# Optimization experiments

Measured on AMD Instinct MI355X. Metric: run time of the kernel, lower is better.

Reference implementation:

```python
import jax, jax.numpy as jnp
import numpy as np

V, D, H, NL, C, CD, B, L = 50257, 512, 8, 4, 10, 64, 16, 512
DH = D // H
EPS = 1e-5


def layer_norm(x, g, b):
    m = jnp.mean(x, axis=-1, keepdims=True)
    v = jnp.var(x, axis=-1, keepdims=True)
    return (x - m) * jax.lax.rsqrt(v + EPS) * g + b


def setup_inputs() -> dict:
    key = jax.random.key(0)
    ks = jax.random.split(key, 16)
    s = lambda k, shape: (jax.random.normal(k, shape, jnp.float32) * 0.02)
    x = jax.random.randint(ks[0], (B, L), 0, V, dtype=jnp.int32)
    return {
        "x": x,
        "embed": s(ks[1], (V, D)),
        "pos": jax.random.normal(ks[2], (1, L, D), jnp.float32),  # nn.Parameter randn
        "Wqkv": s(ks[3], (NL, 3 * D, D)), "bqkv": jnp.zeros((NL, 3 * D)),
        "Wo": s(ks[4], (NL, D, D)), "bo": jnp.zeros((NL, D)),
        "ln1_g": jnp.ones((NL, D)), "ln1_b": jnp.zeros((NL, D)),
        "W1": s(ks[5], (NL, 4 * D, D)), "b1": jnp.zeros((NL, 4 * D)),
        "W2": s(ks[6], (NL, D, 4 * D)), "b2": jnp.zeros((NL, D)),
        "ln2_g": jnp.ones((NL, D)), "ln2_b": jnp.zeros((NL, D)),
        "cnt_ln_g": jnp.ones((V,)), "cnt_ln_b": jnp.zeros((V,)),
        "Wc": s(ks[7], (CD, V)), "bc": jnp.zeros((CD,)),
        "Wh": s(ks[8], (C, D + CD)), "bh": jnp.zeros((C,)),
    }


def _encoder(x, embed, pos, Wqkv, bqkv, Wo, bo, ln1_g, ln1_b, W1, b1, W2, b2, ln2_g, ln2_b):
    h = embed[x] + pos[:, : x.shape[1]]  # (B,L,D)
    scale = 1.0 / jnp.sqrt(jnp.float32(DH))
    for i in range(NL):
        # post-LN TransformerEncoderLayer, gelu (exact), dropout=0 (eval)
        qkv = h @ Wqkv[i].T + bqkv[i]
        q, k, v = jnp.split(qkv, 3, axis=-1)
        q = q.reshape(B, L, H, DH)
        k = k.reshape(B, L, H, DH)
        v = v.reshape(B, L, H, DH)
        att = jax.nn.softmax(jnp.einsum("bqhd,bkhd->bhqk", q, k) * scale, axis=-1)
        o = jnp.einsum("bhqk,bkhd->bqhd", att, v).reshape(B, L, D)
        h = layer_norm(h + o @ Wo[i].T + bo[i], ln1_g[i], ln1_b[i])
        ff = jax.nn.gelu(h @ W1[i].T + b1[i], approximate=False) @ W2[i].T + b2[i]
        h = layer_norm(h + ff, ln2_g[i], ln2_b[i])
    return h


def reference(x, embed, pos, Wqkv, bqkv, Wo, bo, ln1_g, ln1_b, W1, b1, W2, b2,
              ln2_g, ln2_b, cnt_ln_g, cnt_ln_b, Wc, bc, Wh, bh):
    enc = _encoder(x, embed, pos, Wqkv, bqkv, Wo, bo, ln1_g, ln1_b, W1, b1, W2, b2, ln2_g, ln2_b)
    ctx_vec = enc.mean(axis=1)  # (B,D)
    # histogram of tokens per sequence, pad (id 0) excluded: same math as
    # one_hot(x).masked_fill(x==pad).sum(1) but O(B*L) scatter-add.
    mask = (x != 0).astype(jnp.float32)
    counts = jnp.zeros((B, V), jnp.float32).at[jnp.arange(B)[:, None], x].add(mask)
    cf = jax.nn.relu(layer_norm(counts, cnt_ln_g, cnt_ln_b) @ Wc.T + bc)  # (B,CD)
    feat = jnp.concatenate([ctx_vec, cf], axis=-1)
    return feat @ Wh.T + bh  # (B,C)
```

## Files before the change

kernel.cpp:

```cpp
#include <hip/hip_runtime.h>
#include <hip/hip_bf16.h>
#include <math.h>

#define V_  50257
#define D_  512
#define H_  8
#define NL_ 4
#define C_  10
#define CD_ 64
#define B_  16
#define L_  512
#define DH_ 64

typedef __attribute__((ext_vector_type(8))) short bf16x8;
typedef __attribute__((ext_vector_type(4))) float f32x4;

__device__ inline float bf2f(unsigned short u) {
    union { unsigned int i; float f; } c; c.i = ((unsigned int)u) << 16; return c.f;
}
__device__ inline unsigned short f2bf(float f) {
    unsigned int x = __float_as_uint(f);
    unsigned int r = (x + 0x7fffu + ((x >> 16) & 1u)) >> 16;
    return (unsigned short)r;
}
__device__ inline unsigned long long pack4(float a, float b, float c, float d) {
    return (unsigned long long)f2bf(a)         |
           ((unsigned long long)f2bf(b) << 16) |
           ((unsigned long long)f2bf(c) << 32) |
           ((unsigned long long)f2bf(d) << 48);
}

__device__ inline void gload16(const unsigned short* g, unsigned short* l) {
    __builtin_amdgcn_global_load_lds(
        (const __attribute__((address_space(1))) unsigned int*)g,
        (__attribute__((address_space(3))) unsigned int*)l,
        16, 0, 0);
}

template<int BM, int BN, int WGM, int WGN, int EPI>
__global__ __launch_bounds__(256) void gemm_bf16(
    const unsigned short* __restrict__ A, int lda, long aHi, long aLo,
    const unsigned short* __restrict__ B, int ldb, long bHi, long bLo,
    void* __restrict__ Cout, int ldc, long cHi, long cLo,
    const float* __restrict__ bias,
    const unsigned short* __restrict__ resb, int ldr,
    int K, unsigned short* __restrict__ vtout)
{
    constexpr int BK = 64;
    constexpr int FM = BM / (WGM * 16);
    constexpr int FN = BN / (WGN * 16);
    constexpr int CHA = BM / 8;
    constexpr int CHB = BN / 8;
    extern __shared__ unsigned short glds[];
    unsigned short* As = glds;
    unsigned short* Bs = glds + 2 * BM * BK;

    const int z  = blockIdx.z;
    const int zh = z >> 3, zl = z & 7;
    A += zh * aHi + zl * aLo;
    B += zh * bHi + zl * bLo;
    const long coff = zh * cHi + zl * cLo;

    const int tid  = threadIdx.x;
    const int lane = tid & 63;
    const int w    = tid >> 6;
    const int wr   = w / WGN, wc = w % WGN;
    const long rowA0 = (long)blockIdx.x * BM;
    const long rowB0 = (long)blockIdx.y * BN;

    f32x4 acc[FM][FN];
    #pragma unroll
    for (int m = 0; m < FM; m++)
        #pragma unroll
        for (int n = 0; n < FN; n++)
            #pragma unroll
            for (int r = 0; r < 4; r++) acc[m][n][r] = 0.f;

    const int lr   = lane & 15;
    const int crow = lane >> 3;
    const int ccol = ((lane & 7) ^ crow) * 8;

    auto stage = [&](int bf, int k0) {
        #pragma unroll
        for (int c0 = 0; c0 < CHA / 4; c0++) {
            const int c = c0 * 4 + w;
            gload16(&A[(rowA0 + c * 8 + crow) * (long)lda + k0 + ccol],
                    &As[bf * BM * BK + c * 512]);
        }
        #pragma unroll
        for (int c0 = 0; c0 < CHB / 4; c0++) {
            const int c = c0 * 4 + w;
            gload16(&B[(rowB0 + c * 8 + crow) * (long)ldb + k0 + ccol],
                    &Bs[bf * BN * BK + c * 512]);
        }
    };

    stage(0, 0);
    int cur = 0;
    for (int k0 = 0; k0 < K; k0 += BK) {
        __syncthreads();
        if (k0 + BK < K) stage(cur ^ 1, k0 + BK);

        #pragma unroll
        for (int kh = 0; kh < 2; kh++) {
            bf16x8 af[FM], bfr[FN];
            const int sl = ((kh * 4 + (lane >> 4)) ^ (lr & 7)) * 8;
            #pragma unroll
            for (int m = 0; m < FM; m++)
                af[m] = *(const bf16x8*)
                    &As[cur * BM * BK + (wr * FM * 16 + m * 16 + lr) * BK + sl];
            #pragma unroll
            for (int n = 0; n < FN; n++)
                bfr[n] = *(const bf16x8*)
                    &Bs[cur * BN * BK + (wc * FN * 16 + n * 16 + lr) * BK + sl];
            #pragma unroll
            for (int m = 0; m < FM; m++)
                #pragma unroll
                for (int n = 0; n < FN; n++)
                    acc[m][n] = __builtin_amdgcn_mfma_f32_16x16x32_bf16(
                        af[m], bfr[n], acc[m][n], 0, 0, 0);
        }
        cur ^= 1;
    }

    const int rg = (lane >> 4) * 4;
    if constexpr (EPI == 4) {
        if (rowB0 >= 2 * D_) {
            unsigned short* T = glds;
            __syncthreads();
            #pragma unroll
            for (int m = 0; m < FM; m++)
                #pragma unroll
                for (int n = 0; n < FN; n++) {
                    const int lcol = wc * FN * 16 + n * 16 + lr;
                    const float bv = bias[(int)rowB0 + lcol];
                    #pragma unroll
                    for (int r = 0; r < 4; r++) {
                        const int lrow = wr * FM * 16 + m * 16 + rg + r;
                        T[lrow * 132 + lcol] = f2bf(acc[m][n][r] + bv);
                    }
                }
            __syncthreads();
            const int bb = (int)(rowA0 >> 9);
            const int l0 = (int)(rowA0 & 511);
            const int vcBase = (int)(rowB0 - 2 * D_);
            for (int c = tid; c < 2048; c += 256) {
                const int vc    = c & 127;
                const int ch    = c >> 7;
                const int lt2   = ch >> 3;
                const int gslot = ch & 7;
                const int gvc = vcBase + vc;
                const int hd = gvc >> 6, d = gvc & 63;
                bf16x8 o;
                #pragma unroll
                for (int j = 0; j < 8; j++)
                    o[j] = (short)T[(lt2 * 64 + gslot * 8 + j) * 132 + vc];
                *(bf16x8*)&vtout[(long)(bb * 8 + hd) * (DH_ * L_)
                                 + (long)d * 512 + l0 + lt2 * 64
                                 + ((gslot ^ (d & 7)) * 8)] = o;
            }
            return;
        }
        #pragma unroll
        for (int m = 0; m < FM; m++)
            #pragma unroll
            for (int n = 0; n < FN; n++) {
                const int col = (int)rowB0 + wc * FN * 16 + n * 16 + lr;
                const float bv = bias[col];
                #pragma unroll
                for (int r = 0; r < 4; r++) {
                    const long row = rowA0 + wr * FM * 16 + m * 16 + rg + r;
                    ((unsigned short*)Cout)[row * ldc + col] =
                        f2bf(acc[m][n][r] + bv);
                }
            }
        return;
    }

    #pragma unroll
    for (int m = 0; m < FM; m++) {
        #pragma unroll
        for (int n = 0; n < FN; n++) {
            const int col = (int)rowB0 + wc * FN * 16 + n * 16 + lr;
            const float bv = bias ? bias[col] : 0.f;
            #pragma unroll
            for (int r = 0; r < 4; r++) {
                const long row = rowA0 + wr * FM * 16 + m * 16 + rg + r;
                float v = acc[m][n][r] + bv;
                const long o = coff + row * ldc + col;
                if constexpr (EPI == 0) {
                    ((unsigned short*)Cout)[o] = f2bf(v);
                } else if constexpr (EPI == 3) {
                    ((unsigned short*)Cout)[o] =
                        f2bf(v + bf2f(resb[row * ldr + col]));
                } else {
                    float g = 0.5f * v * (1.f + erff(v * 0.70710678118f));
                    ((unsigned short*)Cout)[o] = f2bf(g);
                }
            }
        }
    }
}

__global__ __launch_bounds__(256) void attn_kernel(
    const unsigned short* __restrict__ qkv,
    const unsigned short* __restrict__ vt,
    unsigned short* __restrict__ attno)
{
    extern __shared__ unsigned short lds[];
    unsigned short* Qs = lds;
    unsigned short* Ks = lds + 4096;
    unsigned short* Ps = lds + 4096;
    unsigned short* Vb = lds + 20480;

    const int bid = blockIdx.x;
    const int z   = bid & 127;
    const int qb  = bid >> 7;
    const int b = z >> 3, hh = z & 7;
    const unsigned short* Q  = qkv + (long)b * (L_ * 3 * D_) + hh * DH_;
    const unsigned short* Kp = Q + D_;
    const int row0 = qb * 64;

    const int tid = threadIdx.x, lane = tid & 63, w = tid >> 6;
    const int lr = lane & 15, lg = lane >> 4;

    const int srow = lane >> 3;
    const int scol = ((lane & 7) ^ (srow & 7)) * 8;
    #pragma unroll
    for (int c = 0; c < 2; c++)
        gload16(&Q[(long)(row0 + (w * 2 + c) * 8 + srow) * (3 * D_) + scol],
                &Qs[(w * 2 + c) * 512]);
    #pragma unroll
    for (int c = 0; c < 16; c++)
        gload16(&Kp[(long)((c * 4 + w) * 8 + srow) * (3 * D_) + scol],
                &Ks[(c * 4 + w) * 512]);
    __syncthreads();

    f32x4 acc[32];
    #pragma unroll
    for (int n = 0; n < 32; n++)
        #pragma unroll
        for (int r = 0; r < 4; r++) acc[n][r] = 0.f;

    __builtin_amdgcn_s_setprio(1);
    #pragma unroll
    for (int ks = 0; ks < 2; ks++) {
        const int sl = ((ks * 4 + lg) ^ (lr & 7)) * 8;
        bf16x8 qf = *(const bf16x8*)&Qs[(w * 16 + lr) * 64 + sl];
        #pragma unroll
        for (int n = 0; n < 32; n++) {
            bf16x8 kf = *(const bf16x8*)&Ks[(n * 16 + lr) * 64 + sl];
            acc[n] = __builtin_amdgcn_mfma_f32_16x16x32_bf16(kf, qf, acc[n], 0, 0, 0);
        }
    }
    __builtin_amdgcn_s_setprio(0);

    constexpr float scale = 0.125f;
    float red[32];
    #pragma unroll
    for (int n = 0; n < 32; n++)
        red[n] = fmaxf(fmaxf(acc[n][0], acc[n][1]), fmaxf(acc[n][2], acc[n][3]));
    #pragma unroll
    for (int st = 16; st; st >>= 1)
        #pragma unroll
        for (int i = 0; i < 16; i++)
            if (i < st) red[i] = fmaxf(red[i], red[i + st]);
    float mx = red[0];
    mx = fmaxf(mx, __shfl_xor(mx, 16));
    mx = fmaxf(mx, __shfl_xor(mx, 32));
    const float ms = mx * scale;
    #pragma unroll
    for (int n = 0; n < 32; n++) {
        float e0 = __expf(acc[n][0] * scale - ms);
        float e1 = __expf(acc[n][1] * scale - ms);
        float e2 = __expf(acc[n][2] * scale - ms);
        float e3 = __expf(acc[n][3] * scale - ms);
        acc[n][0] = e0; acc[n][1] = e1; acc[n][2] = e2; acc[n][3] = e3;
        red[n] = (e0 + e1) + (e2 + e3);
    }
    #pragma unroll
    for (int st = 16; st; st >>= 1)
        #pragma unroll
        for (int i = 0; i < 16; i++)
            if (i < st) red[i] += red[i + st];
    float s = red[0];
    s += __shfl_xor(s, 16);
    s += __shfl_xor(s, 32);
    const float rinv = 1.f / s;

    __syncthreads();

    const long vbase = (long)z * (DH_ * L_);
    const int vrow2 = lane >> 5;
    const int vs    = lane & 31;
    const int q     = w * 16 + lr;
    f32x4 accO[4];
    #pragma unroll
    for (int dt = 0; dt < 4; dt++)
        #pragma unroll
        for (int r = 0; r < 4; r++) accO[dt][r] = 0.f;

    #pragma unroll
    for (int hf = 0; hf < 2; hf++) {
        if (hf) __syncthreads();
        #pragma unroll
        for (int c = 0; c < 8; c++) {
            const int ch = c * 4 + w;
            const int dloc = ch * 2 + vrow2;
            gload16(&vt[vbase + (long)dloc * 512 + hf * 256 + vs * 8],
                    &Vb[ch * 512]);
        }
        #pragma unroll
        for (int n = 0; n < 16; n++) {
            const int slot = (n * 2 + (lg >> 1)) ^ (lr & 7);
            unsigned long long pk = pack4(acc[hf * 16 + n][0], acc[hf * 16 + n][1],
                                          acc[hf * 16 + n][2], acc[hf * 16 + n][3]);
            *(unsigned long long*)&Ps[q * 256 + slot * 8 + (lg & 1) * 4] = pk;
        }
        __syncthreads();
        __builtin_amdgcn_s_setprio(1);
        #pragma unroll
        for (int kstep = 0; kstep < 8; kstep++) {
            const int sl = ((kstep * 4 + lg) ^ (lr & 7)) * 8;
            bf16x8 pf = *(const bf16x8*)&Ps[q * 256 + sl];
            #pragma unroll
            for (int dt = 0; dt < 4; dt++) {
                bf16x8 vf = *(const bf16x8*)&Vb[(dt * 16 + lr) * 256 + sl];
                accO[dt] = __builtin_amdgcn_mfma_f32_16x16x32_bf16(vf, pf, accO[dt], 0, 0, 0);
            }
        }
        __builtin_amdgcn_s_setprio(0);
    }

    unsigned short* op = attno + (long)(b * L_ + row0 + q) * D_ + hh * DH_;
    #pragma unroll
    for (int dt = 0; dt < 4; dt++) {
        unsigned long long pk = pack4(accO[dt][0] * rinv, accO[dt][1] * rinv,
                                      accO[dt][2] * rinv, accO[dt][3] * rinv);
        *(unsigned long long*)&op[dt * 16 + lg * 4] = pk;
    }
}

__global__ __launch_bounds__(256) void cvtall_kernel(
    const float* __restrict__ s0, const float* __restrict__ s1,
    const float* __restrict__ s2, const float* __restrict__ s3,
    unsigned short* __restrict__ dst)
{
    const long n0 = 786432, n1 = 262144, n2 = 1048576;
    long i4 = (long)blockIdx.x * 256 + threadIdx.x;
    const float* s; long off;
    if (i4 < n0)                { s = s0; off = 0; }
    else if (i4 < n0 + n1)      { s = s1; off = n0; }
    else if (i4 < n0 + n1 + n2) { s = s2; off = n0 + n1; }
    else                        { s = s3; off = n0 + n1 + n2; }
    float4 v = ((const float4*)s)[i4 - off];
    *(unsigned long long*)&dst[i4 * 4] = pack4(v.x, v.y, v.z, v.w);
}

__global__ __launch_bounds__(256) void embed_kernel(
    const int* __restrict__ x, const float* __restrict__ emb,
    const float* __restrict__ pos, unsigned short* __restrict__ hb)
{
    const long row = blockIdx.x;
    const int tok = x[row];
    const int l = (int)(row & (L_ - 1));
    const int d0 = threadIdx.x * 2;
    float2 e = *(const float2*)&emb[(long)tok * D_ + d0];
    float2 p = *(const float2*)&pos[(long)l * D_ + d0];
    float a0 = e.x + p.x, a1 = e.y + p.y;
    unsigned int pk = (unsigned int)f2bf(a0) | ((unsigned int)f2bf(a1) << 16);
    *(unsigned int*)&hb[row * D_ + d0] = pk;
}

__global__ __launch_bounds__(256) void ln_kernel(
    const unsigned short* __restrict__ t, const float* __restrict__ g,
    const float* __restrict__ bb, unsigned short* __restrict__ hb)
{
    const int lane = threadIdx.x & 63;
    const long row = (long)blockIdx.x * 4 + (threadIdx.x >> 6);
    const unsigned short* x = t + row * D_;
    float v[8];
    bf16x8 d = *(const bf16x8*)&x[lane * 8];
    #pragma unroll
    for (int j = 0; j < 8; j++) v[j] = bf2f((unsigned short)d[j]);
    float s = 0.f;
    #pragma unroll
    for (int j = 0; j < 8; j++) s += v[j];
    #pragma unroll
    for (int o = 32; o; o >>= 1) s += __shfl_xor(s, o);
    const float m = s * (1.f / D_);
    float q = 0.f;
    #pragma unroll
    for (int j = 0; j < 8; j++) { float dd = v[j] - m; q += dd * dd; }
    #pragma unroll
    for (int o = 32; o; o >>= 1) q += __shfl_xor(q, o);
    const float rr = rsqrtf(q * (1.f / D_) + 1e-5f);
    bf16x8 ob;
    #pragma unroll
    for (int j = 0; j < 8; j++) {
        int dd = lane * 8 + j;
        ob[j] = (short)f2bf((v[j] - m) * rr * g[dd] + bb[dd]);
    }
    *(bf16x8*)&hb[row * D_ + lane * 8] = ob;
}

__global__ __launch_bounds__(512) void ctxmean_kernel(
    const unsigned short* __restrict__ hb, float* __restrict__ ctx)
{
    const int b = blockIdx.x, seg = blockIdx.y;
    const int d = threadIdx.x;
    float s = 0.f;
    #pragma unroll 4
    for (int l = seg * 64; l < seg * 64 + 64; l++)
        s += bf2f(hb[((long)b * L_ + l) * D_ + d]);
    atomicAdd(&ctx[b * D_ + d], s * (1.f / L_));
}

__global__ __launch_bounds__(256) void zero_kernel(float* __restrict__ p, long n)
{
    long i = (long)blockIdx.x * 256 + threadIdx.x;
    if (i < n) p[i] = 0.f;
}

__global__ __launch_bounds__(256) void zscat_kernel(
    const int* __restrict__ x, float* __restrict__ counts)
{
    const int i = blockIdx.x * 256 + threadIdx.x;
    if (i >= B_ * L_) return;
    const int tok = x[i];
    if (tok != 0) counts[(long)(i >> 9) * V_ + tok] = 0.f;
}

__global__ __launch_bounds__(256) void hist_kernel(
    const int* __restrict__ x, float* __restrict__ counts)
{
    const int i = blockIdx.x * 256 + threadIdx.x;
    if (i >= B_ * L_) return;
    const int tok = x[i];
    if (tok != 0) atomicAdd(&counts[(long)(i >> 9) * V_ + tok], 1.0f);
}

__global__ __launch_bounds__(512) void cstats_kernel(
    const int* __restrict__ x, const float* __restrict__ counts,
    float* __restrict__ statsraw)
{
    const int b = blockIdx.x, t = threadIdx.x;
    const int tok = x[b * L_ + t];
    float s1 = 0.f, s2 = 0.f;
    if (tok != 0) { s1 = 1.f; s2 = counts[(long)b * V_ + tok]; }
    #pragma unroll
    for (int o = 32; o; o >>= 1) { s1 += __shfl_xor(s1, o); s2 += __shfl_xor(s2, o); }
    __shared__ float r1[8], r2[8];
    if ((t & 63) == 0) { r1[t >> 6] = s1; r2[t >> 6] = s2; }
    __syncthreads();
    if (t == 0) {
        float t1 = 0.f, t2 = 0.f;
        #pragma unroll
        for (int i = 0; i < 8; i++) { t1 += r1[i]; t2 += r2[i]; }
        statsraw[b * 2] = t1;
        statsraw[b * 2 + 1] = t2;
    }
}

__global__ __launch_bounds__(256) void wct_kernel(
    const float* __restrict__ Wc, const float* __restrict__ g,
    float* __restrict__ WcT)
{
    __shared__ float tile[64][65];
    __shared__ float gs[64];
    const int v0 = blockIdx.x * 64;
    const int t = threadIdx.x;
    if (t < 64) gs[t] = (v0 + t < V_) ? g[v0 + t] : 0.f;
    const int vv = t & 63;
    const int vg = v0 + vv;
    #pragma unroll
    for (int r = 0; r < 16; r++) {
        int cd = r * 4 + (t >> 6);
        tile[cd][vv] = (vg < V_) ? Wc[(long)cd * V_ + vg] : 0.f;
    }
    __syncthreads();
    #pragma unroll
    for (int r = 0; r < 16; r++) {
        int v2 = r * 4 + (t >> 6);
        int cd = t & 63;
        if (v0 + v2 < V_)
            WcT[(long)(v0 + v2) * 64 + cd] = tile[cd][v2] * gs[v2];
    }
}

__global__ __launch_bounds__(256) void sgbred_kernel(
    const float* __restrict__ Wc, const float* __restrict__ g,
    const float* __restrict__ bb, float* __restrict__ sgb)
{
    const int cd = blockIdx.x >> 2, chunk = blockIdx.x & 3;
    const int n0 = chunk * 12565;
    const int n1 = min(n0 + 12565, V_);
    float s1 = 0.f, s2 = 0.f;
    for (int v = n0 + threadIdx.x; v < n1; v += 256) {
        float wv = Wc[(long)cd * V_ + v];
        s1 += wv * g[v];
        s2 += wv * bb[v];
    }
    #pragma unroll
    for (int o = 32; o; o >>= 1) { s1 += __shfl_xor(s1, o); s2 += __shfl_xor(s2, o); }
    __shared__ float r1[4], r2[4];
    if ((threadIdx.x & 63) == 0) { r1[threadIdx.x >> 6] = s1; r2[threadIdx.x >> 6] = s2; }
    __syncthreads();
    if (threadIdx.x == 0) {
        atomicAdd(&sgb[cd * 2],     r1[0] + r1[1] + r1[2] + r1[3]);
        atomicAdd(&sgb[cd * 2 + 1], r2[0] + r2[1] + r2[2] + r2[3]);
    }
}

__global__ __launch_bounds__(256) void cgather_kernel(
    const int* __restrict__ x, const float* __restrict__ WcT,
    float* __restrict__ dot)
{
    const int b = blockIdx.x, seg = blockIdx.y;
    const int wv = threadIdx.x >> 6, lane = threadIdx.x & 63;
    float s = 0.f;
    #pragma unroll
    for (int i = 0; i < 16; i++) {
        int tok = x[b * L_ + seg * 64 + wv * 16 + i];
        if (tok != 0) s += WcT[(long)tok * 64 + lane];
    }
    atomicAdd(&dot[b * 64 + lane], s);
}

__global__ void cfinal_kernel(
    const float* __restrict__ dot, const float* __restrict__ statsraw,
    const float* __restrict__ sgb, const float* __restrict__ bc,
    float* __restrict__ cf)
{
    const int b = blockIdx.x, cd = threadIdx.x;
    const float s1 = statsraw[b * 2], s2 = statsraw[b * 2 + 1];
    const float m = s1 * (1.f / V_);
    const float r = rsqrtf(s2 * (1.f / V_) - m * m + 1e-5f);
    float v = r * (dot[b * 64 + cd] - m * sgb[cd * 2]) + sgb[cd * 2 + 1] + bc[cd];
    cf[b * CD_ + cd] = fmaxf(v, 0.f);
}

__global__ __launch_bounds__(256) void final_kernel(
    const float* __restrict__ ctx, const float* __restrict__ cf,
    const float* __restrict__ Wh, const float* __restrict__ bh,
    float* __restrict__ out)
{
    const int p = threadIdx.x;
    if (p >= B_ * C_) return;
    const int b = p / C_, c = p % C_;
    float s = bh[c];
    const float* wrow = Wh + (long)c * (D_ + CD_);
    for (int d = 0; d < D_; d++) s += ctx[b * D_ + d] * wrow[d];
    for (int j = 0; j < CD_; j++) s += cf[b * CD_ + j] * wrow[D_ + j];
    out[p] = s;
}

extern "C" void kernel_launch(void* const* d_in, const int* in_sizes, int n_in,
                              void* d_out, int out_size, void* d_ws, size_t ws_size,
                              hipStream_t stream)
{
    const int*   x      = (const int*)  d_in[0];
    const float* embedw = (const float*)d_in[1];
    const float* pos    = (const float*)d_in[2];
    const float* Wqkv   = (const float*)d_in[3];
    const float* bqkv   = (const float*)d_in[4];
    const float* Wo     = (const float*)d_in[5];
    const float* bo     = (const float*)d_in[6];
    const float* ln1g   = (const float*)d_in[7];
    const float* ln1b   = (const float*)d_in[8];
    const float* W1     = (const float*)d_in[9];
    const float* b1     = (const float*)d_in[10];
    const float* W2     = (const float*)d_in[11];
    const float* b2     = (const float*)d_in[12];
    const float* ln2g   = (const float*)d_in[13];
    const float* ln2b   = (const float*)d_in[14];
    const float* cgv    = (const float*)d_in[15];
    const float* cbv    = (const float*)d_in[16];
    const float* Wc     = (const float*)d_in[17];
    const float* bc     = (const float*)d_in[18];
    const float* Wh     = (const float*)d_in[19];
    const float* bh     = (const float*)d_in[20];
    float* out = (float*)d_out;

    char* ws = (char*)d_ws;
    size_t off = 0;
    auto alloc = [&](size_t bytes) -> void* {
        void* p = ws + off;
        off += (bytes + 255) & ~(size_t)255;
        return p;
    };
    unsigned short* hb    = (unsigned short*)alloc((size_t)B_ * L_ * D_ * 2);
    unsigned short* qkv   = (unsigned short*)alloc((size_t)B_ * L_ * 3 * D_ * 2);
    unsigned short* vt    = (unsigned short*)alloc((size_t)B_ * H_ * DH_ * L_ * 2);
    unsigned short* ff1   = (unsigned short*)alloc((size_t)B_ * L_ * 4 * D_ * 2);
    unsigned short* attno = (unsigned short*)alloc((size_t)B_ * L_ * D_ * 2);
    unsigned short* tbuf  = (unsigned short*)alloc((size_t)B_ * L_ * D_ * 2);
    unsigned short* wqb   = (unsigned short*)alloc((size_t)NL_ * 3 * D_ * D_ * 2);
    unsigned short* wob   = (unsigned short*)alloc((size_t)NL_ * D_ * D_ * 2);
    unsigned short* w1b   = (unsigned short*)alloc((size_t)NL_ * 4 * D_ * D_ * 2);
    unsigned short* w2b   = (unsigned short*)alloc((size_t)NL_ * 4 * D_ * D_ * 2);
    float*          counts= (float*)alloc((size_t)B_ * V_ * 4);
    float*          statsraw = (float*)alloc(B_ * 2 * 4);
    float*          sgb   = (float*)alloc(CD_ * 2 * 4);
    float*          dot   = (float*)alloc(B_ * CD_ * 4);
    float*          ctx   = (float*)alloc(B_ * D_ * 4);
    float*          cf    = (float*)alloc(B_ * CD_ * 4);
    float*          WcT   = (float*)qkv;

    cvtall_kernel<<<12288, 256, 0, stream>>>(Wqkv, Wo, W1, W2, wqb);

    embed_kernel<<<B_*L_, 256, 0, stream>>>(x, embedw, pos, hb);

    const int lds_128 = (128 + 128) * 64 * 4;
    const int lds_64  = (64 + 128) * 64 * 4;

    for (int i = 0; i < NL_; i++) {
        gemm_bf16<128,128,2,2,4><<<dim3(64,12,1),256,lds_128,stream>>>(
            hb, 512, 0, 0,
            wqb + (size_t)i*786432, 512, 0, 0,
            qkv, 1536, 0, 0,
            bqkv + i*1536, nullptr, 0, 512, vt);
        attn_kernel<<<1024, 256, 73728, stream>>>(qkv, vt, attno);
        gemm_bf16<64,128,1,4,3><<<dim3(128,4,1),256,lds_64,stream>>>(
            attno, 512, 0, 0,
            wob + (size_t)i*262144, 512, 0, 0,
            tbuf, 512, 0, 0,
            bo + i*512, hb, 512, 512, nullptr);
        ln_kernel<<<2048,256,0,stream>>>(tbuf, ln1g + i*512, ln1b + i*512, hb);
        gemm_bf16<128,128,2,2,2><<<dim3(64,16,1),256,lds_128,stream>>>(
            hb, 512, 0, 0,
            w1b + (size_t)i*1048576, 512, 0, 0,
            ff1, 2048, 0, 0,
            b1 + i*2048, nullptr, 0, 512, nullptr);
        gemm_bf16<64,128,1,4,3><<<dim3(128,4,1),256,lds_64,stream>>>(
            ff1, 2048, 0, 0,
            w2b + (size_t)i*1048576, 2048, 0, 0,
            tbuf, 512, 0, 0,
            b2 + i*512, hb, 512, 2048, nullptr);
        ln_kernel<<<2048,256,0,stream>>>(tbuf, ln2g + i*512, ln2b + i*512, hb);
    }

    {
        long span = (((char*)cf + ((B_*CD_*4 + 255) & ~255)) - (char*)statsraw) / 4;
        zero_kernel<<<(span + 255)/256, 256, 0, stream>>>(statsraw, span);
    }
    zscat_kernel<<<(B_*L_ + 255)/256, 256, 0, stream>>>(x, counts);
    ctxmean_kernel<<<dim3(B_,8),512,0,stream>>>(hb, ctx);
    hist_kernel<<<(B_*L_ + 255)/256, 256, 0, stream>>>(x, counts);
    cstats_kernel<<<B_,512,0,stream>>>(x, counts, statsraw);
    wct_kernel<<<(V_ + 63)/64, 256, 0, stream>>>(Wc, cgv, WcT);
    sgbred_kernel<<<256,256,0,stream>>>(Wc, cgv, cbv, sgb);
    cgather_kernel<<<dim3(B_,8),256,0,stream>>>(x, WcT, dot);
    cfinal_kernel<<<B_,64,0,stream>>>(dot, statsraw, sgb, bc, cf);
    final_kernel<<<1,256,0,stream>>>(ctx, cf, Wh, bh, out);
}
```

Before: 670.7 us.

## Switch GEMM to triple-buffered BK=32 pipeline with explicit vmcnt barriers

Rewrites the bf16 GEMM main loop to use three LDS stages with a K-tile of 32 instead of double buffering with a K-tile of 64. Loads are issued two tiles ahead, and a hand-written s_waitcnt vmcnt(N) plus s_barrier waits only for the oldest stage. The LDS swizzle is reworked to match the narrower tile, and LDS allocation shrinks, which could allow more blocks per CU. In exchange there are more loop iterations and barriers per K, and correctness now depends on the hard-coded vmcnt counts matching the number of loads each wave issues per stage.

```diff
diff --git a/kernel.cpp b/kernel.cpp
--- a/kernel.cpp
+++ b/kernel.cpp
@@ -37,6 +37,15 @@
         16, 0, 0);
 }
 
+template<int N> __device__ inline void wait_barrier() {
+    if constexpr (N == 0)
+        asm volatile("s_waitcnt vmcnt(0) lgkmcnt(0)\n\ts_barrier" ::: "memory");
+    else if constexpr (N == 3)
+        asm volatile("s_waitcnt vmcnt(3) lgkmcnt(0)\n\ts_barrier" ::: "memory");
+    else
+        asm volatile("s_waitcnt vmcnt(4) lgkmcnt(0)\n\ts_barrier" ::: "memory");
+}
+
 template<int BM, int BN, int WGM, int WGN, int EPI>
 __global__ __launch_bounds__(256) void gemm_bf16(
     const unsigned short* __restrict__ A, int lda, long aHi, long aLo,
@@ -46,14 +55,13 @@
     const unsigned short* __restrict__ resb, int ldr,
     int K, unsigned short* __restrict__ vtout)
 {
-    constexpr int BK = 64;
+    constexpr int BK = 32;
     constexpr int FM = BM / (WGM * 16);
     constexpr int FN = BN / (WGN * 16);
-    constexpr int CHA = BM / 8;
-    constexpr int CHB = BN / 8;
+    constexpr int CHA = BM / 16;
+    constexpr int CHB = BN / 16;
+    constexpr int LPW = (CHA + CHB) / 4;
     extern __shared__ unsigned short glds[];
-    unsigned short* As = glds;
-    unsigned short* Bs = glds + 2 * BM * BK;
 
     const int z  = blockIdx.z;
     const int zh = z >> 3, zl = z & 7;
@@ -77,50 +85,50 @@
             for (int r = 0; r < 4; r++) acc[m][n][r] = 0.f;
 
     const int lr   = lane & 15;
-    const int crow = lane >> 3;
-    const int ccol = ((lane & 7) ^ crow) * 8;
+    const int crow = lane >> 2;
+    const int ccol = ((lane & 3) ^ ((crow >> 1) & 3)) * 8;
+    const int lks  = ((lane >> 4) ^ ((lr >> 1) & 3)) * 8;
 
     auto stage = [&](int bf, int k0) {
         #pragma unroll
         for (int c0 = 0; c0 < CHA / 4; c0++) {
             const int c = c0 * 4 + w;
-            gload16(&A[(rowA0 + c * 8 + crow) * (long)lda + k0 + ccol],
-                    &As[bf * BM * BK + c * 512]);
+            gload16(&A[(rowA0 + c * 16 + crow) * (long)lda + k0 + ccol],
+                    &glds[bf * BM * BK + c * 512]);
         }
         #pragma unroll
         for (int c0 = 0; c0 < CHB / 4; c0++) {
             const int c = c0 * 4 + w;
-            gload16(&B[(rowB0 + c * 8 + crow) * (long)ldb + k0 + ccol],
-                    &Bs[bf * BN * BK + c * 512]);
+            gload16(&B[(rowB0 + c * 16 + crow) * (long)ldb + k0 + ccol],
+                    &glds[3 * BM * BK + bf * BN * BK + c * 512]);
         }
     };
 
+    const int nt = K / BK;
     stage(0, 0);
-    int cur = 0;
-    for (int k0 = 0; k0 < K; k0 += BK) {
-        __syncthreads();
-        if (k0 + BK < K) stage(cur ^ 1, k0 + BK);
-
-        #pragma unroll
-        for (int kh = 0; kh < 2; kh++) {
-            bf16x8 af[FM], bfr[FN];
-            const int sl = ((kh * 4 + (lane >> 4)) ^ (lr & 7)) * 8;
-            #pragma unroll
-            for (int m = 0; m < FM; m++)
-                af[m] = *(const bf16x8*)
-                    &As[cur * BM * BK + (wr * FM * 16 + m * 16 + lr) * BK + sl];
+    stage(1, BK);
+    for (int t = 0; t < nt; ++t) {
+        if (t + 1 < nt) wait_barrier<LPW>();
+        else            wait_barrier<0>();
+        if (t + 2 < nt) stage((t + 2) % 3, (t + 2) * BK);
+
+        const int cur = t % 3;
+        bf16x8 af[FM], bfr[FN];
+        #pragma unroll
+        for (int m = 0; m < FM; m++)
+            af[m] = *(const bf16x8*)
+                &glds[cur * BM * BK + (wr * FM * 16 + m * 16 + lr) * BK + lks];
+        #pragma unroll
+        for (int n = 0; n < FN; n++)
+            bfr[n] = *(const bf16x8*)
+                &glds[3 * BM * BK + cur * BN * BK
+                      + (wc * FN * 16 + n * 16 + lr) * BK + lks];
+        #pragma unroll
+        for (int m = 0; m < FM; m++)
             #pragma unroll
             for (int n = 0; n < FN; n++)
-                bfr[n] = *(const bf16x8*)
-                    &Bs[cur * BN * BK + (wc * FN * 16 + n * 16 + lr) * BK + sl];
-            #pragma unroll
-            for (int m = 0; m < FM; m++)
-                #pragma unroll
-                for (int n = 0; n < FN; n++)
-                    acc[m][n] = __builtin_amdgcn_mfma_f32_16x16x32_bf16(
-                        af[m], bfr[n], acc[m][n], 0, 0, 0);
-        }
-        cur ^= 1;
+                acc[m][n] = __builtin_amdgcn_mfma_f32_16x16x32_bf16(
+                    af[m], bfr[n], acc[m][n], 0, 0, 0);
     }
 
     const int rg = (lane >> 4) * 4;
@@ -611,8 +619,8 @@
 
     embed_kernel<<<B_*L_, 256, 0, stream>>>(x, embedw, pos, hb);
 
-    const int lds_128 = (128 + 128) * 64 * 4;
-    const int lds_64  = (64 + 128) * 64 * 4;
+    const int lds_128 = 3 * (128 + 128) * 32 * 2;
+    const int lds_64  = 3 * (64 + 128) * 32 * 2;
 
     for (int i = 0; i < NL_; i++) {
         gemm_bf16<128,128,2,2,4><<<dim3(64,12,1),256,lds_128,stream>>>(
```

Measured after the change: 707.2 us (median of 2 runs). 5.4% more time.
